# Optimization experiments

Hardware: AMD Instinct MI355X
Metric: run time of the kernel (lower is better)

The kernel has to match this reference:

```python
import jax, jax.numpy as jnp
import numpy as np

N_NODES = 50000
N_EDGES = 1_600_000
IN_DIM, HID_DIM, OUT_DIM = 128, 128, 64


def setup_inputs() -> dict:
    key = jax.random.key(0)
    k_x, k_e, k_w1, k_b1, k_w2, k_b2 = jax.random.split(key, 6)
    x = jax.random.normal(k_x, (N_NODES, IN_DIM), dtype=jnp.float32)
    edge_index = jax.random.randint(k_e, (2, N_EDGES), 0, N_NODES)
    # Learned params (PyG GCNConv: linear weight + bias per layer)
    W1 = jax.random.normal(k_w1, (IN_DIM, HID_DIM), dtype=jnp.float32) * (1.0 / np.sqrt(IN_DIM))
    b1 = jax.random.normal(k_b1, (HID_DIM,), dtype=jnp.float32) * 0.02
    W2 = jax.random.normal(k_w2, (HID_DIM, OUT_DIM), dtype=jnp.float32) * (1.0 / np.sqrt(HID_DIM))
    b2 = jax.random.normal(k_b2, (OUT_DIM,), dtype=jnp.float32) * 0.02
    return {"x": x, "edge_index": edge_index, "W1": W1, "b1": b1, "W2": W2, "b2": b2}


def _gcn_conv(x, W, b, src, dst, norm, n):
    # x: [N, d_in]; transform first (d small), then gather-scale-scatter over edges.
    xw = x @ W                                   # [N, d_out]
    msg = xw[src] * norm[:, None]                # [E+N, d_out] gathered messages
    out = jax.ops.segment_sum(msg, dst, num_segments=n)
    return out + b


def reference(x, edge_index, W1, b1, W2, b2):
    n = x.shape[0]
    # GCN normalization with self-loops: A_hat = D^-1/2 (A + I) D^-1/2
    loop = jnp.arange(n, dtype=edge_index.dtype)
    src = jnp.concatenate([edge_index[0], loop])
    dst = jnp.concatenate([edge_index[1], loop])
    deg = jnp.zeros((n,), x.dtype).at[dst].add(1.0)
    dinv = jnp.where(deg > 0, jax.lax.rsqrt(deg), 0.0)
    norm = dinv[src] * dinv[dst]                 # [E+N]
    h = _gcn_conv(x, W1, b1, src, dst, norm, n)
    h = jax.nn.relu(h)
    # F.dropout(training=self.training): eval mode -> identity
    out = _gcn_conv(h, W2, b2, src, dst, norm, n)
    return out
```

## Files before the change

kernel.cpp:

```cpp
#include <hip/hip_runtime.h>
#include <cstddef>

#define MAXB 512
#define BSHIFT 7
#define ACHUNK 8192

typedef __attribute__((ext_vector_type(8))) short short8;
typedef __attribute__((ext_vector_type(4))) float f32x4;

__device__ inline unsigned pack_bf16x2(float a, float b) {
    unsigned ua = __float_as_uint(a), ub = __float_as_uint(b);
    ua = (ua + 0x7FFFu + ((ua >> 16) & 1u)) >> 16;
    ub = (ub + 0x7FFFu + ((ub >> 16) & 1u)) >> 16;
    return ua | (ub << 16);
}
__device__ inline unsigned short bf16rne(float f) {
    unsigned u = __float_as_uint(f);
    return (unsigned short)((u + 0x7FFFu + ((u >> 16) & 1u)) >> 16);
}
__device__ inline float bf_lo(unsigned u) { return __uint_as_float(u << 16); }
__device__ inline float bf_hi(unsigned u) { return __uint_as_float(u & 0xFFFF0000u); }

__device__ inline void nt_store4(const float4& v, float* p) {
    f32x4 t = { v.x, v.y, v.z, v.w };
    __builtin_nontemporal_store(t, (f32x4*)p);
}

__global__ __launch_bounds__(512) void k_zero512(int* __restrict__ p) {
    p[threadIdx.x] = 0;
}

__global__ __launch_bounds__(256) void k_histA(const int* __restrict__ dst, int* __restrict__ bcnt,
                                               int E, int nbuck) {
    __shared__ int hist[MAXB];
    const int tid = threadIdx.x;
    const int e0  = blockIdx.x * ACHUNK;
    const int e1  = min(e0 + ACHUNK, E);
    for (int i = tid; i < nbuck; i += 256) hist[i] = 0;
    __syncthreads();
    for (int e = e0 + tid; e < e1; e += 256)
        atomicAdd(&hist[dst[e] >> BSHIFT], 1);
    __syncthreads();
    for (int i = tid; i < nbuck; i += 256)
        if (hist[i]) atomicAdd(&bcnt[i], hist[i]);
}

__global__ __launch_bounds__(512) void k_bscan(const int* __restrict__ bcnt, int* __restrict__ bstart,
                                               int* __restrict__ bcur) {
    __shared__ int sh[512];
    const int t = threadIdx.x;
    int v = bcnt[t];
    sh[t] = v;
    __syncthreads();
    for (int d = 1; d < 512; d <<= 1) {
        int u = (t >= d) ? sh[t - d] : 0;
        __syncthreads();
        sh[t] += u;
        __syncthreads();
    }
    int ex = sh[t] - v;
    bstart[t] = ex;
    bcur[t]   = ex;
}

__global__ __launch_bounds__(256) void k_passA(const int* __restrict__ src, const int* __restrict__ dst,
                                               int* __restrict__ bcur, int2* __restrict__ tmp,
                                               int E, int nbuck) {
    __shared__ int hist[MAXB];
    __shared__ int gbase[MAXB];
    const int tid = threadIdx.x;
    const int e0  = blockIdx.x * ACHUNK;
    const int e1  = min(e0 + ACHUNK, E);
    for (int i = tid; i < nbuck; i += 256) hist[i] = 0;
    __syncthreads();
    for (int e = e0 + tid; e < e1; e += 256)
        atomicAdd(&hist[dst[e] >> BSHIFT], 1);
    __syncthreads();
    for (int i = tid; i < nbuck; i += 256) {
        int c = hist[i];
        gbase[i] = c ? atomicAdd(&bcur[i], c) : 0;
        hist[i] = 0;
    }
    __syncthreads();
    for (int e = e0 + tid; e < e1; e += 256) {
        int d = dst[e];
        int b = d >> BSHIFT;
        int slot = atomicAdd(&hist[b], 1);
        tmp[gbase[b] + slot] = make_int2(src[e], d);
    }
}

__global__ __launch_bounds__(256) void k_passB(const int2* __restrict__ tmp, const int* __restrict__ bstart,
                                               const int* __restrict__ bcnt, int* __restrict__ deg,
                                               float* __restrict__ dinv, int* __restrict__ off,
                                               int* __restrict__ esrc, int N) {
    __shared__ int cnt[1 << BSHIFT];
    __shared__ int loff[1 << BSHIFT];
    __shared__ int cur[1 << BSHIFT];
    const int b     = blockIdx.x;
    const int tid   = threadIdx.x;
    const int node0 = b << BSHIFT;
    const int base  = bstart[b];
    const int cntB  = bcnt[b];

    if (tid < 128) cnt[tid] = 0;
    __syncthreads();
    for (int i = tid; i < cntB; i += 256)
        atomicAdd(&cnt[tmp[base + i].y - node0], 1);
    __syncthreads();
    if (tid < 128) loff[tid] = cnt[tid];
    __syncthreads();
    for (int d = 1; d < 128; d <<= 1) {
        int u = (tid >= d && tid < 128) ? loff[tid - d] : 0;
        __syncthreads();
        if (tid < 128) loff[tid] += u;
        __syncthreads();
    }
    if (tid < 128) {
        int c  = cnt[tid];
        int ex = loff[tid] - c;
        cur[tid] = ex;
        if (node0 + tid < N) {
            deg [node0 + tid] = c + 1;
            dinv[node0 + tid] = rsqrtf((float)(c + 1));
            off [node0 + tid] = base + ex;
        }
    }
    __syncthreads();
    for (int i = tid; i < cntB; i += 256) {
        int2 ent = tmp[base + i];
        int  pos = atomicAdd(&cur[ent.y - node0], 1);
        esrc[base + pos] = ent.x;
    }
}

__global__ __launch_bounds__(256) void k_gemm1(const float* __restrict__ x, const float* __restrict__ W,
                                               unsigned short* __restrict__ xwb, int M) {
    __shared__ unsigned short Wt[128 * 144];
    __shared__ unsigned short outS[64 * 128];
    const int tid  = threadIdx.x;
    const int row0 = blockIdx.x * 64;

    for (int i = tid; i < 128 * 128; i += 256) {
        int k = i >> 7, col = i & 127;
        Wt[col * 144 + k] = bf16rne(W[i]);
    }
    __syncthreads();

    const int w  = tid >> 6, l = tid & 63;
    const int lr = l & 15,  kg = l >> 4;
    const int row = row0 + w * 16 + lr;

    f32x4 zero4 = {0.f, 0.f, 0.f, 0.f};
    f32x4 acc[8];
#pragma unroll
    for (int ct = 0; ct < 8; ++ct) acc[ct] = zero4;

#pragma unroll
    for (int ks = 0; ks < 4; ++ks) {
        uint4 aw = make_uint4(0u, 0u, 0u, 0u);
        if (row < M) {
            const float* ap = x + (size_t)row * 128 + ks * 32 + kg * 8;
            float4 u = *(const float4*)ap;
            float4 v = *(const float4*)(ap + 4);
            aw = make_uint4(pack_bf16x2(u.x, u.y), pack_bf16x2(u.z, u.w),
                            pack_bf16x2(v.x, v.y), pack_bf16x2(v.z, v.w));
        }
        short8 afrag = *(short8*)&aw;
#pragma unroll
        for (int ct = 0; ct < 8; ++ct) {
            short8 bfrag = *(const short8*)&Wt[(ct * 16 + lr) * 144 + ks * 32 + kg * 8];
            acc[ct] = __builtin_amdgcn_mfma_f32_16x16x32_bf16(afrag, bfrag, acc[ct], 0, 0, 0);
        }
    }

#pragma unroll
    for (int ct = 0; ct < 8; ++ct)
#pragma unroll
        for (int q = 0; q < 4; ++q)
            outS[(w * 16 + kg * 4 + q) * 128 + ct * 16 + lr] = bf16rne(acc[ct][q]);
    __syncthreads();

    for (int i = 0; i < 4; ++i) {
        int idx = i * 256 + tid;
        int r   = idx >> 4;
        if (row0 + r < M)
            ((uint4*)xwb)[(size_t)row0 * 16 + idx] = ((const uint4*)outS)[idx];
    }
}

__global__ __launch_bounds__(256) void k_gemm2(const float* __restrict__ h_in, const float* __restrict__ W,
                                               unsigned short* __restrict__ hwb, int M) {
    __shared__ unsigned short Wt[64 * 144];
    __shared__ unsigned short outS[64 * 64];
    const int tid  = threadIdx.x;
    const int row0 = blockIdx.x * 64;

    for (int i = tid; i < 128 * 64; i += 256) {
        int k = i >> 6, col = i & 63;
        Wt[col * 144 + k] = bf16rne(W[i]);
    }
    __syncthreads();

    const int w  = tid >> 6, l = tid & 63;
    const int lr = l & 15,  kg = l >> 4;
    const int row = row0 + w * 16 + lr;

    f32x4 zero4 = {0.f, 0.f, 0.f, 0.f};
    f32x4 acc[4];
#pragma unroll
    for (int ct = 0; ct < 4; ++ct) acc[ct] = zero4;

#pragma unroll
    for (int ks = 0; ks < 4; ++ks) {
        uint4 aw = make_uint4(0u, 0u, 0u, 0u);
        if (row < M) {
            const float* ap = h_in + (size_t)row * 128 + ks * 32 + kg * 8;
            float4 u = *(const float4*)ap;
            float4 v = *(const float4*)(ap + 4);
            u.x = fmaxf(u.x, 0.f); u.y = fmaxf(u.y, 0.f); u.z = fmaxf(u.z, 0.f); u.w = fmaxf(u.w, 0.f);
            v.x = fmaxf(v.x, 0.f); v.y = fmaxf(v.y, 0.f); v.z = fmaxf(v.z, 0.f); v.w = fmaxf(v.w, 0.f);
            aw = make_uint4(pack_bf16x2(u.x, u.y), pack_bf16x2(u.z, u.w),
                            pack_bf16x2(v.x, v.y), pack_bf16x2(v.z, v.w));
        }
        short8 afrag = *(short8*)&aw;
#pragma unroll
        for (int ct = 0; ct < 4; ++ct) {
            short8 bfrag = *(const short8*)&Wt[(ct * 16 + lr) * 144 + ks * 32 + kg * 8];
            acc[ct] = __builtin_amdgcn_mfma_f32_16x16x32_bf16(afrag, bfrag, acc[ct], 0, 0, 0);
        }
    }

#pragma unroll
    for (int ct = 0; ct < 4; ++ct)
#pragma unroll
        for (int q = 0; q < 4; ++q)
            outS[(w * 16 + kg * 4 + q) * 64 + ct * 16 + lr] = bf16rne(acc[ct][q]);
    __syncthreads();

    for (int i = 0; i < 2; ++i) {
        int idx = i * 256 + tid;
        int r   = idx >> 3;
        if (row0 + r < M)
            ((uint4*)hwb)[(size_t)row0 * 8 + idx] = ((const uint4*)outS)[idx];
    }
}

__global__ __launch_bounds__(256) void k_agg1(const uint2* __restrict__ xwb, const int* __restrict__ esrc,
                                              const int* __restrict__ off, const int* __restrict__ deg,
                                              const float* __restrict__ dinv, const float* __restrict__ b,
                                              float* __restrict__ out1, int N) {
    const int node = blockIdx.x * 4 + (threadIdx.x >> 6);
    if (node >= N) return;
    const int lane = threadIdx.x & 63;
    const int half = lane >> 5;
    const int lc   = lane & 31;
    const int c0   = lc << 2;

    const float di = dinv[node];
    float4 acc0 = {0,0,0,0}, acc1 = {0,0,0,0}, acc2 = {0,0,0,0}, acc3 = {0,0,0,0};
    if (half == 0) {
        float w0 = di * di;
        uint2  sv = xwb[(size_t)node * 32 + lc];
        float4 bb = *(const float4*)&b[c0];
        acc0.x = bb.x + bf_lo(sv.x) * w0; acc0.y = bb.y + bf_hi(sv.x) * w0;
        acc0.z = bb.z + bf_lo(sv.y) * w0; acc0.w = bb.w + bf_hi(sv.y) * w0;
    }

    const int base = off[node];
    const int cnt  = deg[node] - 1;
    for (int p0 = 0; p0 < cnt; p0 += 64) {
        int   es = 0;
        float ew = 0.f;
        if (p0 + lane < cnt) {
            es = __builtin_nontemporal_load(&esrc[base + p0 + lane]);
            ew = dinv[es] * di;
        }
        const int take = min(64, cnt - p0);
        int j = 0;
        for (; j + 16 <= take; j += 16) {
            int i0 = j + half,      i1 = j + 2 + half,  i2 = j + 4 + half,  i3 = j + 6 + half;
            int i4 = j + 8 + half,  i5 = j + 10 + half, i6 = j + 12 + half, i7 = j + 14 + half;
            int   s0 = __shfl(es, i0); float w0f = __shfl(ew, i0);
            int   s1 = __shfl(es, i1); float w1f = __shfl(ew, i1);
            int   s2 = __shfl(es, i2); float w2f = __shfl(ew, i2);
            int   s3 = __shfl(es, i3); float w3f = __shfl(ew, i3);
            int   s4 = __shfl(es, i4); float w4f = __shfl(ew, i4);
            int   s5 = __shfl(es, i5); float w5f = __shfl(ew, i5);
            int   s6 = __shfl(es, i6); float w6f = __shfl(ew, i6);
            int   s7 = __shfl(es, i7); float w7f = __shfl(ew, i7);
            uint2 v0 = xwb[(size_t)s0 * 32 + lc];
            uint2 v1 = xwb[(size_t)s1 * 32 + lc];
            uint2 v2 = xwb[(size_t)s2 * 32 + lc];
            uint2 v3 = xwb[(size_t)s3 * 32 + lc];
            uint2 v4 = xwb[(size_t)s4 * 32 + lc];
            uint2 v5 = xwb[(size_t)s5 * 32 + lc];
            uint2 v6 = xwb[(size_t)s6 * 32 + lc];
            uint2 v7 = xwb[(size_t)s7 * 32 + lc];
            acc0.x += bf_lo(v0.x) * w0f; acc0.y += bf_hi(v0.x) * w0f;
            acc0.z += bf_lo(v0.y) * w0f; acc0.w += bf_hi(v0.y) * w0f;
            acc1.x += bf_lo(v1.x) * w1f; acc1.y += bf_hi(v1.x) * w1f;
            acc1.z += bf_lo(v1.y) * w1f; acc1.w += bf_hi(v1.y) * w1f;
            acc2.x += bf_lo(v2.x) * w2f; acc2.y += bf_hi(v2.x) * w2f;
            acc2.z += bf_lo(v2.y) * w2f; acc2.w += bf_hi(v2.y) * w2f;
            acc3.x += bf_lo(v3.x) * w3f; acc3.y += bf_hi(v3.x) * w3f;
            acc3.z += bf_lo(v3.y) * w3f; acc3.w += bf_hi(v3.y) * w3f;
            acc0.x += bf_lo(v4.x) * w4f; acc0.y += bf_hi(v4.x) * w4f;
            acc0.z += bf_lo(v4.y) * w4f; acc0.w += bf_hi(v4.y) * w4f;
            acc1.x += bf_lo(v5.x) * w5f; acc1.y += bf_hi(v5.x) * w5f;
            acc1.z += bf_lo(v5.y) * w5f; acc1.w += bf_hi(v5.y) * w5f;
            acc2.x += bf_lo(v6.x) * w6f; acc2.y += bf_hi(v6.x) * w6f;
            acc2.z += bf_lo(v6.y) * w6f; acc2.w += bf_hi(v6.y) * w6f;
            acc3.x += bf_lo(v7.x) * w7f; acc3.y += bf_hi(v7.x) * w7f;
            acc3.z += bf_lo(v7.y) * w7f; acc3.w += bf_hi(v7.y) * w7f;
        }
        for (; j + 8 <= take; j += 8) {
            int i0 = j + half, i1 = j + 2 + half, i2 = j + 4 + half, i3 = j + 6 + half;
            int   s0 = __shfl(es, i0); float w0f = __shfl(ew, i0);
            int   s1 = __shfl(es, i1); float w1f = __shfl(ew, i1);
            int   s2 = __shfl(es, i2); float w2f = __shfl(ew, i2);
            int   s3 = __shfl(es, i3); float w3f = __shfl(ew, i3);
            uint2 v0 = xwb[(size_t)s0 * 32 + lc];
            uint2 v1 = xwb[(size_t)s1 * 32 + lc];
            uint2 v2 = xwb[(size_t)s2 * 32 + lc];
            uint2 v3 = xwb[(size_t)s3 * 32 + lc];
            acc0.x += bf_lo(v0.x) * w0f; acc0.y += bf_hi(v0.x) * w0f;
            acc0.z += bf_lo(v0.y) * w0f; acc0.w += bf_hi(v0.y) * w0f;
            acc1.x += bf_lo(v1.x) * w1f; acc1.y += bf_hi(v1.x) * w1f;
            acc1.z += bf_lo(v1.y) * w1f; acc1.w += bf_hi(v1.y) * w1f;
            acc2.x += bf_lo(v2.x) * w2f; acc2.y += bf_hi(v2.x) * w2f;
            acc2.z += bf_lo(v2.y) * w2f; acc2.w += bf_hi(v2.y) * w2f;
            acc3.x += bf_lo(v3.x) * w3f; acc3.y += bf_hi(v3.x) * w3f;
            acc3.z += bf_lo(v3.y) * w3f; acc3.w += bf_hi(v3.y) * w3f;
        }
        for (; j < take; j += 2) {
            int i0 = j + half;
            int   s0 = __shfl(es, i0); float w0f = __shfl(ew, i0);
            uint2 v0 = xwb[(size_t)s0 * 32 + lc];
            acc0.x += bf_lo(v0.x) * w0f; acc0.y += bf_hi(v0.x) * w0f;
            acc0.z += bf_lo(v0.y) * w0f; acc0.w += bf_hi(v0.y) * w0f;
        }
    }
    acc0.x += acc1.x + acc2.x + acc3.x;
    acc0.y += acc1.y + acc2.y + acc3.y;
    acc0.z += acc1.z + acc2.z + acc3.z;
    acc0.w += acc1.w + acc2.w + acc3.w;
    acc0.x += __shfl_xor(acc0.x, 32);
    acc0.y += __shfl_xor(acc0.y, 32);
    acc0.z += __shfl_xor(acc0.z, 32);
    acc0.w += __shfl_xor(acc0.w, 32);
    if (half == 0)
        nt_store4(acc0, &out1[(size_t)node * 128 + c0]);
}

__global__ __launch_bounds__(256) void k_agg2(const uint2* __restrict__ hwb, const int* __restrict__ esrc,
                                              const int* __restrict__ off, const int* __restrict__ deg,
                                              const float* __restrict__ dinv, const float* __restrict__ b,
                                              float* __restrict__ out, int N) {
    const int node = blockIdx.x * 4 + (threadIdx.x >> 6);
    if (node >= N) return;
    const int lane = threadIdx.x & 63;
    const int grp  = lane >> 4;
    const int lc   = lane & 15;
    const int c0   = lc << 2;

    const float di = dinv[node];
    float4 acc0 = {0,0,0,0}, acc1 = {0,0,0,0}, acc2 = {0,0,0,0}, acc3 = {0,0,0,0};
    if (grp == 0) {
        float w0 = di * di;
        uint2  sv = hwb[(size_t)node * 16 + lc];
        float4 bb = *(const float4*)&b[c0];
        acc0.x = bb.x + bf_lo(sv.x) * w0; acc0.y = bb.y + bf_hi(sv.x) * w0;
        acc0.z = bb.z + bf_lo(sv.y) * w0; acc0.w = bb.w + bf_hi(sv.y) * w0;
    }

    const int base = off[node];
    const int cnt  = deg[node] - 1;
    for (int p0 = 0; p0 < cnt; p0 += 64) {
        int   es = 0;
        float ew = 0.f;
        if (p0 + lane < cnt) {
            es = __builtin_nontemporal_load(&esrc[base + p0 + lane]);
            ew = dinv[es] * di;
        }
        const int take = min(64, cnt - p0);
        int j = 0;
        for (; j + 32 <= take; j += 32) {
            int i0 = j + grp,      i1 = j + 4 + grp,  i2 = j + 8 + grp,  i3 = j + 12 + grp;
            int i4 = j + 16 + grp, i5 = j + 20 + grp, i6 = j + 24 + grp, i7 = j + 28 + grp;
            int   s0 = __shfl(es, i0); float w0f = __shfl(ew, i0);
            int   s1 = __shfl(es, i1); float w1f = __shfl(ew, i1);
            int   s2 = __shfl(es, i2); float w2f = __shfl(ew, i2);
            int   s3 = __shfl(es, i3); float w3f = __shfl(ew, i3);
            int   s4 = __shfl(es, i4); float w4f = __shfl(ew, i4);
            int   s5 = __shfl(es, i5); float w5f = __shfl(ew, i5);
            int   s6 = __shfl(es, i6); float w6f = __shfl(ew, i6);
            int   s7 = __shfl(es, i7); float w7f = __shfl(ew, i7);
            uint2 v0 = hwb[(size_t)s0 * 16 + lc];
            uint2 v1 = hwb[(size_t)s1 * 16 + lc];
            uint2 v2 = hwb[(size_t)s2 * 16 + lc];
            uint2 v3 = hwb[(size_t)s3 * 16 + lc];
            uint2 v4 = hwb[(size_t)s4 * 16 + lc];
            uint2 v5 = hwb[(size_t)s5 * 16 + lc];
            uint2 v6 = hwb[(size_t)s6 * 16 + lc];
            uint2 v7 = hwb[(size_t)s7 * 16 + lc];
            acc0.x += bf_lo(v0.x) * w0f; acc0.y += bf_hi(v0.x) * w0f;
            acc0.z += bf_lo(v0.y) * w0f; acc0.w += bf_hi(v0.y) * w0f;
            acc1.x += bf_lo(v1.x) * w1f; acc1.y += bf_hi(v1.x) * w1f;
            acc1.z += bf_lo(v1.y) * w1f; acc1.w += bf_hi(v1.y) * w1f;
            acc2.x += bf_lo(v2.x) * w2f; acc2.y += bf_hi(v2.x) * w2f;
            acc2.z += bf_lo(v2.y) * w2f; acc2.w += bf_hi(v2.y) * w2f;
            acc3.x += bf_lo(v3.x) * w3f; acc3.y += bf_hi(v3.x) * w3f;
            acc3.z += bf_lo(v3.y) * w3f; acc3.w += bf_hi(v3.y) * w3f;
            acc0.x += bf_lo(v4.x) * w4f; acc0.y += bf_hi(v4.x) * w4f;
            acc0.z += bf_lo(v4.y) * w4f; acc0.w += bf_hi(v4.y) * w4f;
            acc1.x += bf_lo(v5.x) * w5f; acc1.y += bf_hi(v5.x) * w5f;
            acc1.z += bf_lo(v5.y) * w5f; acc1.w += bf_hi(v5.y) * w5f;
            acc2.x += bf_lo(v6.x) * w6f; acc2.y += bf_hi(v6.x) * w6f;
            acc2.z += bf_lo(v6.y) * w6f; acc2.w += bf_hi(v6.y) * w6f;
            acc3.x += bf_lo(v7.x) * w7f; acc3.y += bf_hi(v7.x) * w7f;
            acc3.z += bf_lo(v7.y) * w7f; acc3.w += bf_hi(v7.y) * w7f;
        }
        for (; j + 16 <= take; j += 16) {
            int i0 = j + grp, i1 = j + 4 + grp, i2 = j + 8 + grp, i3 = j + 12 + grp;
            int   s0 = __shfl(es, i0); float w0f = __shfl(ew, i0);
            int   s1 = __shfl(es, i1); float w1f = __shfl(ew, i1);
            int   s2 = __shfl(es, i2); float w2f = __shfl(ew, i2);
            int   s3 = __shfl(es, i3); float w3f = __shfl(ew, i3);
            uint2 v0 = hwb[(size_t)s0 * 16 + lc];
            uint2 v1 = hwb[(size_t)s1 * 16 + lc];
            uint2 v2 = hwb[(size_t)s2 * 16 + lc];
            uint2 v3 = hwb[(size_t)s3 * 16 + lc];
            acc0.x += bf_lo(v0.x) * w0f; acc0.y += bf_hi(v0.x) * w0f;
            acc0.z += bf_lo(v0.y) * w0f; acc0.w += bf_hi(v0.y) * w0f;
            acc1.x += bf_lo(v1.x) * w1f; acc1.y += bf_hi(v1.x) * w1f;
            acc1.z += bf_lo(v1.y) * w1f; acc1.w += bf_hi(v1.y) * w1f;
            acc2.x += bf_lo(v2.x) * w2f; acc2.y += bf_hi(v2.x) * w2f;
            acc2.z += bf_lo(v2.y) * w2f; acc2.w += bf_hi(v2.y) * w2f;
            acc3.x += bf_lo(v3.x) * w3f; acc3.y += bf_hi(v3.x) * w3f;
            acc3.z += bf_lo(v3.y) * w3f; acc3.w += bf_hi(v3.y) * w3f;
        }
        for (; j < take; j += 4) {
            int i0 = j + grp;
            int   s0 = __shfl(es, i0); float w0f = __shfl(ew, i0);
            uint2 v0 = hwb[(size_t)s0 * 16 + lc];
            acc0.x += bf_lo(v0.x) * w0f; acc0.y += bf_hi(v0.x) * w0f;
            acc0.z += bf_lo(v0.y) * w0f; acc0.w += bf_hi(v0.y) * w0f;
        }
    }
    acc0.x += acc1.x + acc2.x + acc3.x;
    acc0.y += acc1.y + acc2.y + acc3.y;
    acc0.z += acc1.z + acc2.z + acc3.z;
    acc0.w += acc1.w + acc2.w + acc3.w;
    acc0.x += __shfl_xor(acc0.x, 16); acc0.y += __shfl_xor(acc0.y, 16);
    acc0.z += __shfl_xor(acc0.z, 16); acc0.w += __shfl_xor(acc0.w, 16);
    acc0.x += __shfl_xor(acc0.x, 32); acc0.y += __shfl_xor(acc0.y, 32);
    acc0.z += __shfl_xor(acc0.z, 32); acc0.w += __shfl_xor(acc0.w, 32);
    if (lane < 16)
        nt_store4(acc0, &out[(size_t)node * 64 + c0]);
}

extern "C" void kernel_launch(void* const* d_in, const int* in_sizes, int n_in,
                              void* d_out, int out_size, void* d_ws, size_t ws_size,
                              hipStream_t stream) {
    const float* x  = (const float*)d_in[0];
    const int*   ei = (const int*)  d_in[1];
    const float* W1 = (const float*)d_in[2];
    const float* b1 = (const float*)d_in[3];
    const float* W2 = (const float*)d_in[4];
    const float* b2 = (const float*)d_in[5];
    float* out = (float*)d_out;

    const int N = in_sizes[0] / 128;
    const int E = in_sizes[1] / 2;
    const int* src = ei;
    const int* dst = ei + E;
    const int NBUCK = (N + 127) / 128;
    const int NA    = (E + ACHUNK - 1) / ACHUNK;
    const int NG    = (N + 63) / 64;

    char* w = (char*)d_ws;
    int*            deg     = (int*)w;        w += (size_t)N * 4;
    float*          dinv    = (float*)w;      w += (size_t)N * 4;
    int*            off     = (int*)w;        w += (size_t)N * 4;
    int*            bstart  = (int*)w;        w += 512 * 4;
    int*            bcnt    = (int*)w;        w += 512 * 4;
    int*            bcur    = (int*)w;        w += 512 * 4;
    int*            esrc    = (int*)w;        w += (size_t)E * 4;
    unsigned short* xwb     = (unsigned short*)w;  w += (size_t)N * 128 * 2;
    float*          out1    = (float*)w;      w += (size_t)N * 128 * 4;
    unsigned short* hwb     = (unsigned short*)w;
    int2*           tmp     = (int2*)out1;

    k_zero512 <<<1, 512, 0, stream>>>(bcnt);
    k_histA   <<<NA, 256, 0, stream>>>(dst, bcnt, E, NBUCK);
    k_bscan   <<<1, 512, 0, stream>>>(bcnt, bstart, bcur);
    k_passA   <<<NA, 256, 0, stream>>>(src, dst, bcur, tmp, E, NBUCK);
    k_passB   <<<NBUCK, 256, 0, stream>>>(tmp, bstart, bcnt, deg, dinv, off, esrc, N);

    k_gemm1 <<<NG, 256, 0, stream>>>(x, W1, xwb, N);
    k_agg1  <<<(N + 3) / 4, 256, 0, stream>>>((const uint2*)xwb, esrc, off, deg, dinv, b1, out1, N);

    k_gemm2 <<<NG, 256, 0, stream>>>(out1, W2, hwb, N);
    k_agg2  <<<(N + 3) / 4, 256, 0, stream>>>((const uint2*)hwb, esrc, off, deg, dinv, b2, out, N);
}
```

Baseline: 209.7 us.

## Split feature tables into column halves and aggregate each half separately

The GEMM kernels now write their bf16 outputs as two column-half tables, and each aggregation is run as two passes, one per half, with more edges in flight per wavefront. The smaller gathered table (half the bytes per node) is meant to fit better in L2/MALL cache, raising hit rates for the random neighbour gathers. The cost is reading the CSR edge lists and dinv twice and an extra launch per layer, with fewer useful bytes per gather request.

New measurement: 249.6 us. 19.0% more time.

```diff
diff --git a/kernel.cpp b/kernel.cpp
--- a/kernel.cpp
+++ b/kernel.cpp
@@ -135,7 +135,8 @@
 }
 
 __global__ __launch_bounds__(256) void k_gemm1(const float* __restrict__ x, const float* __restrict__ W,
-                                               unsigned short* __restrict__ xwb, int M) {
+                                               unsigned short* __restrict__ xwbA,
+                                               unsigned short* __restrict__ xwbB, int M) {
     __shared__ unsigned short Wt[128 * 144];
     __shared__ unsigned short outS[64 * 128];
     const int tid  = threadIdx.x;
@@ -183,14 +184,18 @@
 
     for (int i = 0; i < 4; ++i) {
         int idx = i * 256 + tid;
-        int r   = idx >> 4;
-        if (row0 + r < M)
-            ((uint4*)xwb)[(size_t)row0 * 16 + idx] = ((const uint4*)outS)[idx];
+        int r   = idx >> 4, q = idx & 15;
+        if (row0 + r < M) {
+            uint4 v = ((const uint4*)outS)[idx];
+            if (q < 8) ((uint4*)xwbA)[(size_t)(row0 + r) * 8 + q]       = v;
+            else       ((uint4*)xwbB)[(size_t)(row0 + r) * 8 + (q - 8)] = v;
+        }
     }
 }
 
 __global__ __launch_bounds__(256) void k_gemm2(const float* __restrict__ h_in, const float* __restrict__ W,
-                                               unsigned short* __restrict__ hwb, int M) {
+                                               unsigned short* __restrict__ hwbA,
+                                               unsigned short* __restrict__ hwbB, int M) {
     __shared__ unsigned short Wt[64 * 144];
     __shared__ unsigned short outS[64 * 64];
     const int tid  = threadIdx.x;
@@ -240,29 +245,32 @@
 
     for (int i = 0; i < 2; ++i) {
         int idx = i * 256 + tid;
-        int r   = idx >> 3;
-        if (row0 + r < M)
-            ((uint4*)hwb)[(size_t)row0 * 8 + idx] = ((const uint4*)outS)[idx];
-    }
-}
-
-__global__ __launch_bounds__(256) void k_agg1(const uint2* __restrict__ xwb, const int* __restrict__ esrc,
-                                              const int* __restrict__ off, const int* __restrict__ deg,
-                                              const float* __restrict__ dinv, const float* __restrict__ b,
-                                              float* __restrict__ out1, int N) {
+        int r   = idx >> 3, q = idx & 7;
+        if (row0 + r < M) {
+            uint4 v = ((const uint4*)outS)[idx];
+            if (q < 4) ((uint4*)hwbA)[(size_t)(row0 + r) * 4 + q]       = v;
+            else       ((uint4*)hwbB)[(size_t)(row0 + r) * 4 + (q - 4)] = v;
+        }
+    }
+}
+
+__global__ __launch_bounds__(256) void k_aggh64(const uint2* __restrict__ tbl, const int* __restrict__ esrc,
+                                                const int* __restrict__ off, const int* __restrict__ deg,
+                                                const float* __restrict__ dinv, const float* __restrict__ b,
+                                                float* __restrict__ out, int N, int colbase) {
     const int node = blockIdx.x * 4 + (threadIdx.x >> 6);
     if (node >= N) return;
     const int lane = threadIdx.x & 63;
-    const int half = lane >> 5;
-    const int lc   = lane & 31;
+    const int grp  = lane >> 4;
+    const int lc   = lane & 15;
     const int c0   = lc << 2;
 
     const float di = dinv[node];
     float4 acc0 = {0,0,0,0}, acc1 = {0,0,0,0}, acc2 = {0,0,0,0}, acc3 = {0,0,0,0};
-    if (half == 0) {
+    if (grp == 0) {
         float w0 = di * di;
-        uint2  sv = xwb[(size_t)node * 32 + lc];
-        float4 bb = *(const float4*)&b[c0];
+        uint2  sv = tbl[(size_t)node * 16 + lc];
+        float4 bb = *(const float4*)&b[colbase + c0];
         acc0.x = bb.x + bf_lo(sv.x) * w0; acc0.y = bb.y + bf_hi(sv.x) * w0;
         acc0.z = bb.z + bf_lo(sv.y) * w0; acc0.w = bb.w + bf_hi(sv.y) * w0;
     }
@@ -278,9 +286,9 @@
         }
         const int take = min(64, cnt - p0);
         int j = 0;
-        for (; j + 16 <= take; j += 16) {
-            int i0 = j + half,      i1 = j + 2 + half,  i2 = j + 4 + half,  i3 = j + 6 + half;
-            int i4 = j + 8 + half,  i5 = j + 10 + half, i6 = j + 12 + half, i7 = j + 14 + half;
+        for (; j + 32 <= take; j += 32) {
+            int i0 = j + grp,      i1 = j + 4 + grp,  i2 = j + 8 + grp,  i3 = j + 12 + grp;
+            int i4 = j + 16 + grp, i5 = j + 20 + grp, i6 = j + 24 + grp, i7 = j + 28 + grp;
             int   s0 = __shfl(es, i0); float w0f = __shfl(ew, i0);
             int   s1 = __shfl(es, i1); float w1f = __shfl(ew, i1);
             int   s2 = __shfl(es, i2); float w2f = __shfl(ew, i2);
@@ -289,14 +297,14 @@
             int   s5 = __shfl(es, i5); float w5f = __shfl(ew, i5);
             int   s6 = __shfl(es, i6); float w6f = __shfl(ew, i6);
             int   s7 = __shfl(es, i7); float w7f = __shfl(ew, i7);
-            uint2 v0 = xwb[(size_t)s0 * 32 + lc];
-            uint2 v1 = xwb[(size_t)s1 * 32 + lc];
-            uint2 v2 = xwb[(size_t)s2 * 32 + lc];
-            uint2 v3 = xwb[(size_t)s3 * 32 + lc];
-            uint2 v4 = xwb[(size_t)s4 * 32 + lc];
-            uint2 v5 = xwb[(size_t)s5 * 32 + lc];
-            uint2 v6 = xwb[(size_t)s6 * 32 + lc];
-            uint2 v7 = xwb[(size_t)s7 * 32 + lc];
+            uint2 v0 = tbl[(size_t)s0 * 16 + lc];
+            uint2 v1 = tbl[(size_t)s1 * 16 + lc];
+            uint2 v2 = tbl[(size_t)s2 * 16 + lc];
+            uint2 v3 = tbl[(size_t)s3 * 16 + lc];
+            uint2 v4 = tbl[(size_t)s4 * 16 + lc];
+            uint2 v5 = tbl[(size_t)s5 * 16 + lc];
+            uint2 v6 = tbl[(size_t)s6 * 16 + lc];
+            uint2 v7 = tbl[(size_t)s7 * 16 + lc];
             acc0.x += bf_lo(v0.x) * w0f; acc0.y += bf_hi(v0.x) * w0f;
             acc0.z += bf_lo(v0.y) * w0f; acc0.w += bf_hi(v0.y) * w0f;
             acc1.x += bf_lo(v1.x) * w1f; acc1.y += bf_hi(v1.x) * w1f;
@@ -314,16 +322,16 @@
             acc3.x += bf_lo(v7.x) * w7f; acc3.y += bf_hi(v7.x) * w7f;
             acc3.z += bf_lo(v7.y) * w7f; acc3.w += bf_hi(v7.y) * w7f;
         }
-        for (; j + 8 <= take; j += 8) {
-            int i0 = j + half, i1 = j + 2 + half, i2 = j + 4 + half, i3 = j + 6 + half;
+        for (; j + 16 <= take; j += 16) {
+            int i0 = j + grp, i1 = j + 4 + grp, i2 = j + 8 + grp, i3 = j + 12 + grp;
             int   s0 = __shfl(es, i0); float w0f = __shfl(ew, i0);
             int   s1 = __shfl(es, i1); float w1f = __shfl(ew, i1);
             int   s2 = __shfl(es, i2); float w2f = __shfl(ew, i2);
             int   s3 = __shfl(es, i3); float w3f = __shfl(ew, i3);
-            uint2 v0 = xwb[(size_t)s0 * 32 + lc];
-            uint2 v1 = xwb[(size_t)s1 * 32 + lc];
-            uint2 v2 = xwb[(size_t)s2 * 32 + lc];
-            uint2 v3 = xwb[(size_t)s3 * 32 + lc];
+            uint2 v0 = tbl[(size_t)s0 * 16 + lc];
+            uint2 v1 = tbl[(size_t)s1 * 16 + lc];
+            uint2 v2 = tbl[(size_t)s2 * 16 + lc];
+            uint2 v3 = tbl[(size_t)s3 * 16 + lc];
             acc0.x += bf_lo(v0.x) * w0f; acc0.y += bf_hi(v0.x) * w0f;
             acc0.z += bf_lo(v0.y) * w0f; acc0.w += bf_hi(v0.y) * w0f;
             acc1.x += bf_lo(v1.x) * w1f; acc1.y += bf_hi(v1.x) * w1f;
@@ -333,10 +341,10 @@
             acc3.x += bf_lo(v3.x) * w3f; acc3.y += bf_hi(v3.x) * w3f;
             acc3.z += bf_lo(v3.y) * w3f; acc3.w += bf_hi(v3.y) * w3f;
         }
-        for (; j < take; j += 2) {
-            int i0 = j + half;
+        for (; j < take; j += 4) {
+            int i0 = j + grp;
             int   s0 = __shfl(es, i0); float w0f = __shfl(ew, i0);
-            uint2 v0 = xwb[(size_t)s0 * 32 + lc];
+            uint2 v0 = tbl[(size_t)s0 * 16 + lc];
             acc0.x += bf_lo(v0.x) * w0f; acc0.y += bf_hi(v0.x) * w0f;
             acc0.z += bf_lo(v0.y) * w0f; acc0.w += bf_hi(v0.y) * w0f;
         }
@@ -345,31 +353,31 @@
     acc0.y += acc1.y + acc2.y + acc3.y;
     acc0.z += acc1.z + acc2.z + acc3.z;
     acc0.w += acc1.w + acc2.w + acc3.w;
-    acc0.x += __shfl_xor(acc0.x, 32);
-    acc0.y += __shfl_xor(acc0.y, 32);
-    acc0.z += __shfl_xor(acc0.z, 32);
-    acc0.w += __shfl_xor(acc0.w, 32);
-    if (half == 0)
-        nt_store4(acc0, &out1[(size_t)node * 128 + c0]);
-}
-
-__global__ __launch_bounds__(256) void k_agg2(const uint2* __restrict__ hwb, const int* __restrict__ esrc,
-                                              const int* __restrict__ off, const int* __restrict__ deg,
-                                              const float* __restrict__ dinv, const float* __restrict__ b,
-                                              float* __restrict__ out, int N) {
+    acc0.x += __shfl_xor(acc0.x, 16); acc0.y += __shfl_xor(acc0.y, 16);
+    acc0.z += __shfl_xor(acc0.z, 16); acc0.w += __shfl_xor(acc0.w, 16);
+    acc0.x += __shfl_xor(acc0.x, 32); acc0.y += __shfl_xor(acc0.y, 32);
+    acc0.z += __shfl_xor(acc0.z, 32); acc0.w += __shfl_xor(acc0.w, 32);
+    if (lane < 16)
+        nt_store4(acc0, &out[(size_t)node * 128 + colbase + c0]);
+}
+
+__global__ __launch_bounds__(256) void k_aggh32(const uint2* __restrict__ tbl, const int* __restrict__ esrc,
+                                                const int* __restrict__ off, const int* __restrict__ deg,
+                                                const float* __restrict__ dinv, const float* __restrict__ b,
+                                                float* __restrict__ out, int N, int colbase) {
     const int node = blockIdx.x * 4 + (threadIdx.x >> 6);
     if (node >= N) return;
     const int lane = threadIdx.x & 63;
-    const int grp  = lane >> 4;
-    const int lc   = lane & 15;
+    const int grp  = lane >> 3;
+    const int lc   = lane & 7;
     const int c0   = lc << 2;
 
     const float di = dinv[node];
     float4 acc0 = {0,0,0,0}, acc1 = {0,0,0,0}, acc2 = {0,0,0,0}, acc3 = {0,0,0,0};
     if (grp == 0) {
         float w0 = di * di;
-        uint2  sv = hwb[(size_t)node * 16 + lc];
-        float4 bb = *(const float4*)&b[c0];
+        uint2  sv = tbl[(size_t)node * 8 + lc];
+        float4 bb = *(const float4*)&b[colbase + c0];
         acc0.x = bb.x + bf_lo(sv.x) * w0; acc0.y = bb.y + bf_hi(sv.x) * w0;
         acc0.z = bb.z + bf_lo(sv.y) * w0; acc0.w = bb.w + bf_hi(sv.y) * w0;
     }
@@ -385,9 +393,9 @@
         }
         const int take = min(64, cnt - p0);
         int j = 0;
-        for (; j + 32 <= take; j += 32) {
-            int i0 = j + grp,      i1 = j + 4 + grp,  i2 = j + 8 + grp,  i3 = j + 12 + grp;
-            int i4 = j + 16 + grp, i5 = j + 20 + grp, i6 = j + 24 + grp, i7 = j + 28 + grp;
+        for (; j + 64 <= take; j += 64) {
+            int i0 = j + grp,      i1 = j + 8 + grp,  i2 = j + 16 + grp, i3 = j + 24 + grp;
+            int i4 = j + 32 + grp, i5 = j + 40 + grp, i6 = j + 48 + grp, i7 = j + 56 + grp;
             int   s0 = __shfl(es, i0); float w0f = __shfl(ew, i0);
             int   s1 = __shfl(es, i1); float w1f = __shfl(ew, i1);
             int   s2 = __shfl(es, i2); float w2f = __shfl(ew, i2);
@@ -396,14 +404,14 @@
             int   s5 = __shfl(es, i5); float w5f = __shfl(ew, i5);
             int   s6 = __shfl(es, i6); float w6f = __shfl(ew, i6);
             int   s7 = __shfl(es, i7); float w7f = __shfl(ew, i7);
-            uint2 v0 = hwb[(size_t)s0 * 16 + lc];
-            uint2 v1 = hwb[(size_t)s1 * 16 + lc];
-            uint2 v2 = hwb[(size_t)s2 * 16 + lc];
-            uint2 v3 = hwb[(size_t)s3 * 16 + lc];
-            uint2 v4 = hwb[(size_t)s4 * 16 + lc];
-            uint2 v5 = hwb[(size_t)s5 * 16 + lc];
-            uint2 v6 = hwb[(size_t)s6 * 16 + lc];
-            uint2 v7 = hwb[(size_t)s7 * 16 + lc];
+            uint2 v0 = tbl[(size_t)s0 * 8 + lc];
+            uint2 v1 = tbl[(size_t)s1 * 8 + lc];
+            uint2 v2 = tbl[(size_t)s2 * 8 + lc];
+            uint2 v3 = tbl[(size_t)s3 * 8 + lc];
+            uint2 v4 = tbl[(size_t)s4 * 8 + lc];
+            uint2 v5 = tbl[(size_t)s5 * 8 + lc];
+            uint2 v6 = tbl[(size_t)s6 * 8 + lc];
+            uint2 v7 = tbl[(size_t)s7 * 8 + lc];
             acc0.x += bf_lo(v0.x) * w0f; acc0.y += bf_hi(v0.x) * w0f;
             acc0.z += bf_lo(v0.y) * w0f; acc0.w += bf_hi(v0.y) * w0f;
             acc1.x += bf_lo(v1.x) * w1f; acc1.y += bf_hi(v1.x) * w1f;
@@ -421,16 +429,16 @@
             acc3.x += bf_lo(v7.x) * w7f; acc3.y += bf_hi(v7.x) * w7f;
             acc3.z += bf_lo(v7.y) * w7f; acc3.w += bf_hi(v7.y) * w7f;
         }
-        for (; j + 16 <= take; j += 16) {
-            int i0 = j + grp, i1 = j + 4 + grp, i2 = j + 8 + grp, i3 = j + 12 + grp;
+        for (; j + 32 <= take; j += 32) {
+            int i0 = j + grp, i1 = j + 8 + grp, i2 = j + 16 + grp, i3 = j + 24 + grp;
             int   s0 = __shfl(es, i0); float w0f = __shfl(ew, i0);
             int   s1 = __shfl(es, i1); float w1f = __shfl(ew, i1);
             int   s2 = __shfl(es, i2); float w2f = __shfl(ew, i2);
             int   s3 = __shfl(es, i3); float w3f = __shfl(ew, i3);
-            uint2 v0 = hwb[(size_t)s0 * 16 + lc];
-            uint2 v1 = hwb[(size_t)s1 * 16 + lc];
-            uint2 v2 = hwb[(size_t)s2 * 16 + lc];
-            uint2 v3 = hwb[(size_t)s3 * 16 + lc];
+            uint2 v0 = tbl[(size_t)s0 * 8 + lc];
+            uint2 v1 = tbl[(size_t)s1 * 8 + lc];
+            uint2 v2 = tbl[(size_t)s2 * 8 + lc];
+            uint2 v3 = tbl[(size_t)s3 * 8 + lc];
             acc0.x += bf_lo(v0.x) * w0f; acc0.y += bf_hi(v0.x) * w0f;
             acc0.z += bf_lo(v0.y) * w0f; acc0.w += bf_hi(v0.y) * w0f;
             acc1.x += bf_lo(v1.x) * w1f; acc1.y += bf_hi(v1.x) * w1f;
@@ -440,10 +448,10 @@
             acc3.x += bf_lo(v3.x) * w3f; acc3.y += bf_hi(v3.x) * w3f;
             acc3.z += bf_lo(v3.y) * w3f; acc3.w += bf_hi(v3.y) * w3f;
         }
-        for (; j < take; j += 4) {
+        for (; j < take; j += 8) {
             int i0 = j + grp;
             int   s0 = __shfl(es, i0); float w0f = __shfl(ew, i0);
-            uint2 v0 = hwb[(size_t)s0 * 16 + lc];
+            uint2 v0 = tbl[(size_t)s0 * 8 + lc];
             acc0.x += bf_lo(v0.x) * w0f; acc0.y += bf_hi(v0.x) * w0f;
             acc0.z += bf_lo(v0.y) * w0f; acc0.w += bf_hi(v0.y) * w0f;
         }
@@ -452,12 +460,14 @@
     acc0.y += acc1.y + acc2.y + acc3.y;
     acc0.z += acc1.z + acc2.z + acc3.z;
     acc0.w += acc1.w + acc2.w + acc3.w;
+    acc0.x += __shfl_xor(acc0.x, 8);  acc0.y += __shfl_xor(acc0.y, 8);
+    acc0.z += __shfl_xor(acc0.z, 8);  acc0.w += __shfl_xor(acc0.w, 8);
     acc0.x += __shfl_xor(acc0.x, 16); acc0.y += __shfl_xor(acc0.y, 16);
     acc0.z += __shfl_xor(acc0.z, 16); acc0.w += __shfl_xor(acc0.w, 16);
     acc0.x += __shfl_xor(acc0.x, 32); acc0.y += __shfl_xor(acc0.y, 32);
     acc0.z += __shfl_xor(acc0.z, 32); acc0.w += __shfl_xor(acc0.w, 32);
-    if (lane < 16)
-        nt_store4(acc0, &out[(size_t)node * 64 + c0]);
+    if (lane < 8)
+        nt_store4(acc0, &out[(size_t)node * 64 + colbase + c0]);
 }
 
 extern "C" void kernel_launch(void* const* d_in, const int* in_sizes, int n_in,
@@ -478,6 +488,7 @@
     const int NBUCK = (N + 127) / 128;
     const int NA    = (E + ACHUNK - 1) / ACHUNK;
     const int NG    = (N + 63) / 64;
+    const int NAGG  = (N + 3) / 4;
 
     char* w = (char*)d_ws;
     int*            deg     = (int*)w;        w += (size_t)N * 4;
@@ -487,9 +498,11 @@
     int*            bcnt    = (int*)w;        w += 512 * 4;
     int*            bcur    = (int*)w;        w += 512 * 4;
     int*            esrc    = (int*)w;        w += (size_t)E * 4;
-    unsigned short* xwb     = (unsigned short*)w;  w += (size_t)N * 128 * 2;
+    unsigned short* xwbA    = (unsigned short*)w;  w += (size_t)N * 64 * 2;
+    unsigned short* xwbB    = (unsigned short*)w;  w += (size_t)N * 64 * 2;
     float*          out1    = (float*)w;      w += (size_t)N * 128 * 4;
-    unsigned short* hwb     = (unsigned short*)w;
+    unsigned short* hwbA    = (unsigned short*)w;  w += (size_t)N * 32 * 2;
+    unsigned short* hwbB    = (unsigned short*)w;
     int2*           tmp     = (int2*)out1;
 
     k_zero512 <<<1, 512, 0, stream>>>(bcnt);
@@ -498,9 +511,11 @@
     k_passA   <<<NA, 256, 0, stream>>>(src, dst, bcur, tmp, E, NBUCK);
     k_passB   <<<NBUCK, 256, 0, stream>>>(tmp, bstart, bcnt, deg, dinv, off, esrc, N);
 
-    k_gemm1 <<<NG, 256, 0, stream>>>(x, W1, xwb, N);
-    k_agg1  <<<(N + 3) / 4, 256, 0, stream>>>((const uint2*)xwb, esrc, off, deg, dinv, b1, out1, N);
-
-    k_gemm2 <<<NG, 256, 0, stream>>>(out1, W2, hwb, N);
-    k_agg2  <<<(N + 3) / 4, 256, 0, stream>>>((const uint2*)hwb, esrc, off, deg, dinv, b2, out, N);
-}
+    k_gemm1 <<<NG, 256, 0, stream>>>(x, W1, xwbA, xwbB, N);
+    k_aggh64<<<NAGG, 256, 0, stream>>>((const uint2*)xwbA, esrc, off, deg, dinv, b1, out1, N, 0);
+    k_aggh64<<<NAGG, 256, 0, stream>>>((const uint2*)xwbB, esrc, off, deg, dinv, b1, out1, N, 64);
+
+    k_gemm2 <<<NG, 256, 0, stream>>>(out1, W2, hwbA, hwbB, N);
+    k_aggh32<<<NAGG, 256, 0, stream>>>((const uint2*)hwbA, esrc, off, deg, dinv, b2, out, N, 0);
+    k_aggh32<<<NAGG, 256, 0, stream>>>((const uint2*)hwbB, esrc, off, deg, dinv, b2, out, N, 32);
+}
```
